# Optimization experiments

Measured on AMD Instinct MI355X. Metric: run time of the kernel, lower is better.

The kernel has to match this reference:

```python
import jax, jax.numpy as jnp
import numpy as np

DIM = 1024
HEADS = 16
HEAD_DIM = DIM // HEADS
SCALE = HEAD_DIM ** -0.5
KSIZES = (1, 3, 5)


def setup_inputs() -> dict:
    key = jax.random.key(0)
    ks = jax.random.split(key, 16)
    b, n = 2, 2048
    s = 0.02
    inp = {
        "x": jax.random.normal(ks[0], (b, n, DIM), jnp.float32),
        "Wq": jax.random.normal(ks[1], (DIM, DIM), jnp.float32) * s,
        "Wk": jax.random.normal(ks[2], (DIM, DIM), jnp.float32) * s,
        "Wv": jax.random.normal(ks[3], (DIM, DIM), jnp.float32) * s,
        "Wo": jax.random.normal(ks[4], (DIM, DIM), jnp.float32) * s,
        "bo": jnp.zeros((DIM,), jnp.float32),
        "temperature": jnp.ones((1, HEADS, 1, 1), jnp.float32),
        "head_weights": jnp.ones((1, HEADS, 1, 1), jnp.float32),
    }
    # grouped Conv1d kernels: (out_ch=DIM, in_ch_per_group=DIM//HEADS, k)
    for i, k in enumerate(KSIZES):
        inp[f"conv_w{k}"] = jax.random.normal(ks[5 + i], (DIM, DIM // HEADS, k), jnp.float32) * s
        inp[f"conv_b{k}"] = jnp.zeros((DIM,), jnp.float32)
    return inp


def _grouped_conv1d(x_bdn, w, b, k):
    # x_bdn: [b, dim, n]; w: [dim, dim//HEADS, k]; 'same' padding for odd k
    y = jax.lax.conv_general_dilated(
        x_bdn, w, window_strides=(1,), padding=[(k // 2, k // 2)],
        dimension_numbers=("NCH", "OIH", "NCH"), feature_group_count=HEADS)
    return y + b[None, :, None]


def reference(x, Wq, Wk, Wv, Wo, bo, temperature, head_weights,
              conv_w1, conv_b1, conv_w3, conv_b3, conv_w5, conv_b5):
    b, n, _ = x.shape
    split = lambda t: t.reshape(b, n, HEADS, HEAD_DIM).transpose(0, 2, 1, 3)  # b h n d
    q = split(x @ Wq.T)
    k = split(x @ Wk.T)
    v = split(x @ Wv.T)
    dots = jnp.einsum("bhnd,bhmd->bhnm", q, k) * SCALE * temperature
    attn = jax.nn.softmax(dots, axis=-1)
    attn = attn * jax.nn.softmax(head_weights, axis=1)
    out = jnp.einsum("bhnm,bhmd->bhnd", attn, v)
    out = out.transpose(0, 2, 1, 3).reshape(b, n, DIM)  # b n (h d)
    oc = out.transpose(0, 2, 1)  # b dim n
    conv_sum = (_grouped_conv1d(oc, conv_w1, conv_b1, 1)
                + _grouped_conv1d(oc, conv_w3, conv_b3, 3)
                + _grouped_conv1d(oc, conv_w5, conv_b5, 5))
    n_scales = float(len(KSIZES))
    out_combined = out + conv_sum.transpose(0, 2, 1) / n_scales
    return out_combined @ Wo.T + bo
```

## Files before the change

### kernel.cpp

```cpp
#include <hip/hip_runtime.h>

#define DIM 1024
#define HEADS 16
#define HD 64
#define BATCH 2
#define SEQ 2048
#define MROWS (BATCH * SEQ)

typedef short s16x8 __attribute__((ext_vector_type(8)));
typedef short s16x4 __attribute__((ext_vector_type(4)));
typedef float f32x4 __attribute__((ext_vector_type(4)));

__device__ __forceinline__ short f2bf(float f) {
  unsigned u = __builtin_bit_cast(unsigned, f);
  u = u + 0x7fffu + ((u >> 16) & 1u);
  return (short)(u >> 16);
}

__device__ __forceinline__ float bf2f(short s) {
  unsigned u = ((unsigned)(unsigned short)s) << 16;
  return __builtin_bit_cast(float, u);
}

__device__ __forceinline__ float fexp2(float x) { return __builtin_amdgcn_exp2f(x); }

__device__ __forceinline__ unsigned cvtpk(float lo, float hi) {
  unsigned r;
  asm("v_cvt_pk_bf16_f32 %0, %1, %2" : "=v"(r) : "v"(lo), "v"(hi));
  return r;
}

__device__ __forceinline__ void gload16(const void* g, void* l) {
  __builtin_amdgcn_global_load_lds((__attribute__((address_space(1))) void*)g,
                                   (__attribute__((address_space(3))) void*)l,
                                   16, 0, 0);
}

__global__ __launch_bounds__(256) void cvt_bf16(const float* __restrict__ in,
                                                short* __restrict__ out, int n4) {
  int i = blockIdx.x * 256 + threadIdx.x;
  if (i >= n4) return;
  f32x4 v = *(const f32x4*)(in + (size_t)i * 4);
  s16x4 o;
#pragma unroll
  for (int j = 0; j < 4; ++j) o[j] = f2bf(v[j]);
  *(s16x4*)(out + (size_t)i * 4) = o;
}

__global__ __launch_bounds__(256)
void cvt_w4(const float* __restrict__ a, const float* __restrict__ b,
            const float* __restrict__ c, const float* __restrict__ d,
            short* __restrict__ oa, short* __restrict__ ob, short* __restrict__ oc,
            short* __restrict__ od) {
  int k = blockIdx.y;
  const float* in = (k == 0) ? a : (k == 1) ? b : (k == 2) ? c : d;
  short* out = (k == 0) ? oa : (k == 1) ? ob : (k == 2) ? oc : od;
  int i = blockIdx.x * 256 + threadIdx.x;
  f32x4 v = *(const f32x4*)(in + (size_t)i * 4);
  s16x4 o;
#pragma unroll
  for (int j = 0; j < 4; ++j) o[j] = f2bf(v[j]);
  *(s16x4*)(out + (size_t)i * 4) = o;
}

#define QSTAGE(BUF, KT)                                                                \
  _Pragma("unroll") for (int i = 0; i < 2; ++i) {                                      \
    int cbase = i * 512 + wave * 64;                                                   \
    int c = cbase + lane;                                                              \
    int row = c >> 3;                                                                  \
    int cb = ((c ^ row) & 7) << 4;                                                     \
    gload16((const char*)A + ((size_t)(brow + row) * DIM + (KT)) * 2 + cb,             \
            (char*)&As[BUF][0][0] + cbase * 16);                                       \
    gload16((const char*)Bq + ((size_t)(bcol + row) * DIM + (KT)) * 2 + cb,            \
            (char*)&Bs[BUF][0][0][0] + cbase * 16);                                    \
    gload16((const char*)Bk + ((size_t)(bcol + row) * DIM + (KT)) * 2 + cb,            \
            (char*)&Bs[BUF][1][0][0] + cbase * 16);                                    \
    gload16((const char*)Bv + ((size_t)(bcol + row) * DIM + (KT)) * 2 + cb,            \
            (char*)&Bs[BUF][2][0][0] + cbase * 16);                                    \
  }

__global__ __launch_bounds__(512)
void qkv_fused(const short* __restrict__ A, const short* __restrict__ Bq,
               const short* __restrict__ Bk, const short* __restrict__ Bv,
               const float* __restrict__ scq, short* __restrict__ oq,
               short* __restrict__ ok, short* __restrict__ ov) {
  __shared__ __align__(16) short As[2][128][64];
  __shared__ __align__(16) short Bs[2][3][128][64];
  const int tid = threadIdx.x;
  const int lane = tid & 63, wave = tid >> 6;
  const int fr = lane & 15, fg = lane >> 4;
  const int wr = wave >> 1, wc = wave & 1;
  const int brow = blockIdx.y * 128, bcol = blockIdx.x * 128;

  int offA[2][2], offB[2][4];
#pragma unroll
  for (int kk = 0; kk < 2; ++kk) {
    int sw = ((kk * 4 + fg) ^ (fr & 7)) << 4;
#pragma unroll
    for (int m = 0; m < 2; ++m) offA[kk][m] = (wr * 32 + m * 16 + fr) * 128 + sw;
#pragma unroll
    for (int n = 0; n < 4; ++n) offB[kk][n] = (wc * 64 + n * 16 + fr) * 128 + sw;
  }

  f32x4 acc[3][2][4] = {};

  QSTAGE(0, 0);
  __syncthreads();

  for (int kt = 0; kt < DIM; kt += 64) {
    const int cur = (kt >> 6) & 1;
    if (kt + 64 < DIM) { QSTAGE(cur ^ 1, kt + 64); }
    const char* Ab = (const char*)&As[cur][0][0];
    const char* Bb = (const char*)&Bs[cur][0][0][0];
#pragma unroll
    for (int kk = 0; kk < 2; ++kk) {
      s16x8 af[2];
#pragma unroll
      for (int m = 0; m < 2; ++m) af[m] = *(const s16x8*)(Ab + offA[kk][m]);
#pragma unroll
      for (int z = 0; z < 3; ++z) {
        s16x8 bfr[4];
#pragma unroll
        for (int n = 0; n < 4; ++n) bfr[n] = *(const s16x8*)(Bb + z * 16384 + offB[kk][n]);
#pragma unroll
        for (int m = 0; m < 2; ++m)
#pragma unroll
          for (int n = 0; n < 4; ++n)
            acc[z][m][n] =
                __builtin_amdgcn_mfma_f32_16x16x32_bf16(af[m], bfr[n], acc[z][m][n], 0, 0, 0);
      }
    }
    __syncthreads();
  }

  const int hh = (bcol >> 6) + wc;
  const float sv = scq[hh];
#pragma unroll
  for (int m = 0; m < 2; ++m) {
#pragma unroll
    for (int n = 0; n < 4; ++n) {
      int i0 = brow + wr * 32 + m * 16 + fg * 4;
      int dd = n * 16 + fr;
#pragma unroll
      for (int r = 0; r < 4; ++r) {
        int i = i0 + r;
        size_t qko = (((size_t)(i >> 11) * HEADS + hh) * SEQ + (i & (SEQ - 1))) * HD + dd;
        oq[qko] = f2bf(acc[0][m][n][r] * sv);
        ok[qko] = f2bf(acc[1][m][n][r]);
      }
      s16x4 o4;
#pragma unroll
      for (int r = 0; r < 4; ++r) o4[r] = f2bf(acc[2][m][n][r]);
      *(s16x4*)&ov[(((size_t)(i0 >> 11) * HEADS + hh) * HD + dd) * SEQ + (i0 & (SEQ - 1))] = o4;
    }
  }
}

#define GSTAGE(BUF, KT)                                                              \
  _Pragma("unroll") for (int i = 0; i < 4; ++i) {                                    \
    int cbase = (wave * 4 + i) * 64;                                                 \
    int chunk = cbase + lane;                                                        \
    int row = chunk >> 3;                                                            \
    int cb = ((chunk ^ row) & 7) << 4;                                               \
    gload16((const char*)A + ((size_t)(brow + row) * DIM + (KT)) * 2 + cb,           \
            (char*)&As[BUF][0][0] + cbase * 16);                                     \
    gload16((const char*)Bw + ((size_t)(bcol + row) * DIM + (KT)) * 2 + cb,          \
            (char*)&Bs[BUF][0][0] + cbase * 16);                                     \
  }

__global__ __launch_bounds__(256)
void out_gemm(const short* __restrict__ A, const short* __restrict__ Bw,
              const float* __restrict__ bias, float* __restrict__ out) {
  __shared__ __align__(16) short As[2][128][64];
  __shared__ __align__(16) short Bs[2][128][64];
  const int tid = threadIdx.x;
  const int lane = tid & 63, wave = tid >> 6;
  const int fr = lane & 15, fg = lane >> 4;
  const int wr = wave >> 1, wc = wave & 1;
  const int brow = blockIdx.y * 128, bcol = blockIdx.x * 128;
  f32x4 acc[4][4] = {};

  int offA[2][4], offB[2][4];
#pragma unroll
  for (int kk = 0; kk < 2; ++kk)
#pragma unroll
    for (int f = 0; f < 4; ++f) {
      int sw = ((kk * 4 + fg) ^ (fr & 7)) << 4;
      offA[kk][f] = (wr * 64 + f * 16 + fr) * 128 + sw;
      offB[kk][f] = (wc * 64 + f * 16 + fr) * 128 + sw;
    }

  GSTAGE(0, 0);
  __syncthreads();

  for (int kt = 0; kt < DIM; kt += 64) {
    const int cur = (kt >> 6) & 1;
    if (kt + 64 < DIM) { GSTAGE(cur ^ 1, kt + 64); }
    const char* Ab = (const char*)&As[cur][0][0];
    const char* Bb = (const char*)&Bs[cur][0][0];
#pragma unroll
    for (int kk = 0; kk < 2; ++kk) {
      s16x8 af[4], bfr[4];
#pragma unroll
      for (int m = 0; m < 4; ++m) af[m] = *(const s16x8*)(Ab + offA[kk][m]);
#pragma unroll
      for (int n = 0; n < 4; ++n) bfr[n] = *(const s16x8*)(Bb + offB[kk][n]);
#pragma unroll
      for (int m = 0; m < 4; ++m)
#pragma unroll
        for (int n = 0; n < 4; ++n)
          acc[m][n] = __builtin_amdgcn_mfma_f32_16x16x32_bf16(af[m], bfr[n], acc[m][n], 0, 0, 0);
    }
    __syncthreads();
  }

#pragma unroll
  for (int m = 0; m < 4; ++m) {
#pragma unroll
    for (int n = 0; n < 4; ++n) {
      int i0 = brow + wr * 64 + m * 16 + fg * 4;
      int j = bcol + wc * 64 + n * 16 + fr;
#pragma unroll
      for (int r = 0; r < 4; ++r)
        out[(size_t)(i0 + r) * DIM + j] = acc[m][n][r] + bias[j];
    }
  }
}

#define STAGE(BUF, KT)                                                                   \
  gload16((const char*)K + (bhoff + (size_t)((KT) + srow) * HD) * 2 + scs,               \
          (char*)&Ks[BUF][0][0] + wbyte);                                                \
  gload16((const char*)Vt + (vbase + (size_t)srow * SEQ + (KT)) * 2 + scs,               \
          (char*)&Vs[BUF][0][0] + wbyte);

#define ATTN_TILE(CUR, STG, KTSTG, DOSTAGE, WAITSTR)                                     \
  {                                                                                      \
    asm volatile("s_waitcnt " WAITSTR ::: "memory");                                     \
    __builtin_amdgcn_s_barrier();                                                        \
    asm volatile("" ::: "memory");                                                       \
    if (DOSTAGE) { STAGE(STG, KTSTG); }                                                  \
    f32x4 st[4] = {};                                                                    \
    __builtin_amdgcn_s_setprio(1);                                                       \
    _Pragma("unroll") for (int ks = 0; ks < 2; ++ks) {                                   \
      _Pragma("unroll") for (int kf = 0; kf < 4; ++kf) {                                 \
        const s16x8 kfr = *(const s16x8*)((const char*)&Ks[CUR][0][0] + off[ks][kf]);    \
        st[kf] = __builtin_amdgcn_mfma_f32_16x16x32_bf16(kfr, qf_[ks], st[kf], 0, 0, 0); \
      }                                                                                  \
    }                                                                                    \
    __builtin_amdgcn_s_setprio(0);                                                       \
    float rsum = 0.f;                                                                    \
    _Pragma("unroll") for (int kf = 0; kf < 4; ++kf) {                                   \
      float p0 = fexp2(st[kf][0]), p1 = fexp2(st[kf][1]);                                \
      float p2 = fexp2(st[kf][2]), p3 = fexp2(st[kf][3]);                                \
      rsum += (p0 + p1) + (p2 + p3);                                                     \
      uint2 pk;                                                                          \
      pk.x = cvtpk(p0, p1);                                                              \
      pk.y = cvtpk(p2, p3);                                                              \
      *(uint2*)((char*)Psb + pwoff[kf]) = pk;                                            \
    }                                                                                    \
    lrow += rsum;                                                                        \
    __builtin_amdgcn_s_setprio(1);                                                       \
    _Pragma("unroll") for (int ks2 = 0; ks2 < 2; ++ks2) {                                \
      const s16x8 pfr = *(const s16x8*)((const char*)Psb + proff[ks2]);                  \
      _Pragma("unroll") for (int vf = 0; vf < 4; ++vf) {                                 \
        const s16x8 vfr = *(const s16x8*)((const char*)&Vs[CUR][0][0] + off[ks2][vf]);   \
        oacc[vf] = __builtin_amdgcn_mfma_f32_16x16x32_bf16(vfr, pfr, oacc[vf], 0, 0, 0); \
      }                                                                                  \
    }                                                                                    \
    __builtin_amdgcn_s_setprio(0);                                                       \
  }

__global__ __launch_bounds__(512)
void attn_fwd(const short* __restrict__ Q, const short* __restrict__ K,
              const short* __restrict__ Vt, short* __restrict__ att,
              const float* __restrict__ hw) {
  __shared__ __align__(16) short Ks[3][64][64];
  __shared__ __align__(16) short Vs[3][64][64];
  __shared__ __align__(16) short Ps[8][16][72];
  const int bh = blockIdx.y;
  const int h = bh & (HEADS - 1);
  const int qbase = blockIdx.x * 128;
  const int tid = threadIdx.x;
  const int lane = tid & 63, wave = tid >> 6;
  const int fr = lane & 15, fg = lane >> 4;
  const int frx = (fr & 7);

  float hmax = -1e30f;
  for (int i = 0; i < HEADS; ++i) hmax = fmaxf(hmax, hw[i]);
  float hsum = 0.f;
  for (int i = 0; i < HEADS; ++i) hsum += expf(hw[i] - hmax);
  const float hwsm = expf(hw[h] - hmax) / hsum;

  const size_t bhoff = (size_t)bh * SEQ * HD;
  const int qrow = qbase + wave * 16 + fr;
  s16x8 qf_[2];
#pragma unroll
  for (int ks = 0; ks < 2; ++ks)
    qf_[ks] = *(const s16x8*)&Q[bhoff + (size_t)qrow * HD + ks * 32 + fg * 8];

  int off[2][4];
#pragma unroll
  for (int ks = 0; ks < 2; ++ks)
#pragma unroll
    for (int f = 0; f < 4; ++f)
      off[ks][f] = (f * 16 + fr) * 128 + (((ks * 4 + fg) ^ frx) << 4);
  int pwoff[4], proff[2];
#pragma unroll
  for (int kf = 0; kf < 4; ++kf) pwoff[kf] = ((wave * 16 + fr) * 72 + kf * 16 + fg * 4) * 2;
#pragma unroll
  for (int ks2 = 0; ks2 < 2; ++ks2) proff[ks2] = ((wave * 16 + fr) * 72 + ks2 * 32 + fg * 8) * 2;
  const char* Psb = (const char*)&Ps[0][0][0];

  f32x4 oacc[4] = {};
  float lrow = 0.f;

  const int srow = tid >> 3;
  const int scs = ((tid & 7) ^ (srow & 7)) << 4;
  const int wbyte = wave * 64 * 16;
  const size_t vbase = (size_t)bh * HD * SEQ;

  STAGE(0, 0);
  STAGE(1, 64);

  for (int ktg = 0; ktg + 192 <= SEQ; ktg += 192) {
    ATTN_TILE(0, 2, ktg + 128, true, "vmcnt(2)");
    ATTN_TILE(1, 0, ktg + 192, true, "vmcnt(2)");
    ATTN_TILE(2, 1, ktg + 256, true, "vmcnt(2)");
  }
  ATTN_TILE(0, 0, 0, false, "vmcnt(2)");
  ATTN_TILE(1, 0, 0, false, "vmcnt(0)");

  lrow += __shfl_xor(lrow, 16);
  lrow += __shfl_xor(lrow, 32);

  const int b = bh >> 4;
  const float isc = hwsm / lrow;
#pragma unroll
  for (int vf = 0; vf < 4; ++vf) {
    s16x4 o4;
#pragma unroll
    for (int r = 0; r < 4; ++r) o4[r] = f2bf(oacc[vf][r] * isc);
    *(s16x4*)&att[((size_t)b * SEQ + qrow) * DIM + h * HD + vf * 16 + fg * 4] = o4;
  }
}

__global__ __launch_bounds__(256)
void prep_weff(const float* __restrict__ w1, const float* __restrict__ b1,
               const float* __restrict__ w3, const float* __restrict__ b3,
               const float* __restrict__ w5, const float* __restrict__ b5,
               const float* __restrict__ temp, short* __restrict__ weff,
               float* __restrict__ bsum, float* __restrict__ scq) {
  int idx = blockIdx.x * 256 + threadIdx.x;
  if (idx >= DIM * 64) return;
  float t0 = w5[(size_t)idx * 5 + 0];
  float t1 = w5[(size_t)idx * 5 + 1] + w3[(size_t)idx * 3 + 0];
  float t2 = w5[(size_t)idx * 5 + 2] + w3[(size_t)idx * 3 + 1] + w1[idx];
  float t3 = w5[(size_t)idx * 5 + 3] + w3[(size_t)idx * 3 + 2];
  float t4 = w5[(size_t)idx * 5 + 4];
  weff[0 * DIM * 64 + idx] = f2bf(t0);
  weff[1 * DIM * 64 + idx] = f2bf(t1);
  weff[2 * DIM * 64 + idx] = f2bf(t2);
  weff[3 * DIM * 64 + idx] = f2bf(t3);
  weff[4 * DIM * 64 + idx] = f2bf(t4);
  if ((idx & 63) == 0) {
    int o = idx >> 6;
    bsum[o] = b1[o] + b3[o] + b5[o];
  }
  if (idx < HEADS) scq[idx] = 0.125f * temp[idx] * 1.44269504f;
}

#define CP 68
__global__ __launch_bounds__(256)
void conv_mfma(const short* __restrict__ attb, const short* __restrict__ weff,
               const float* __restrict__ bsum, short* __restrict__ comb) {
  __shared__ __align__(16) short As[132][CP];
  __shared__ __align__(16) short Ws[5][64][CP];
  const int b = blockIdx.z, g = blockIdx.y, n0 = blockIdx.x * 128;
  const int tid = threadIdx.x, lane = tid & 63, wave = tid >> 6;
  const int fr = lane & 15, fg = lane >> 4;

  const short* abase = attb + (size_t)b * SEQ * DIM + g * 64;
  for (int idx = tid; idx < 132 * 8; idx += 256) {
    int r = idx >> 3, cb = (idx & 7) * 8;
    int rn = n0 + r - 2;
    s16x8 v = {};
    if (rn >= 0 && rn < SEQ) v = *(const s16x8*)&abase[(size_t)rn * DIM + cb];
    *(s16x8*)&As[r][cb] = v;
  }
  for (int idx = tid; idx < 5 * 64 * 8; idx += 256) {
    int t = idx >> 9;
    int rem = idx & 511;
    int o = rem >> 3, cb = (rem & 7) * 8;
    s16x8 v = *(const s16x8*)&weff[((size_t)t * DIM + g * 64 + o) * 64 + cb];
    *(s16x8*)&Ws[t][o][cb] = v;
  }
  __syncthreads();

  f32x4 acc[2][4] = {};
#pragma unroll
  for (int dt = 0; dt < 5; ++dt) {
#pragma unroll
    for (int kk = 0; kk < 2; ++kk) {
      const int ko = kk * 32 + fg * 8;
      s16x8 af[2], bfr[4];
#pragma unroll
      for (int m = 0; m < 2; ++m)
        af[m] = *(const s16x8*)&As[wave * 32 + m * 16 + fr + dt][ko];
#pragma unroll
      for (int n = 0; n < 4; ++n) bfr[n] = *(const s16x8*)&Ws[dt][n * 16 + fr][ko];
#pragma unroll
      for (int m = 0; m < 2; ++m)
#pragma unroll
        for (int n = 0; n < 4; ++n)
          acc[m][n] = __builtin_amdgcn_mfma_f32_16x16x32_bf16(af[m], bfr[n], acc[m][n], 0, 0, 0);
    }
  }

#pragma unroll
  for (int m = 0; m < 2; ++m) {
#pragma unroll
    for (int n = 0; n < 4; ++n) {
      int lrow0 = wave * 32 + m * 16 + fg * 4;
      int col = n * 16 + fr;
      float bs = bsum[g * 64 + col];
#pragma unroll
      for (int r = 0; r < 4; ++r) {
        int lr = lrow0 + r;
        float res = bf2f(As[lr + 2][col]);
        float outv = res + (acc[m][n][r] + bs) * (1.f / 3.f);
        comb[((size_t)b * SEQ + n0 + lr) * DIM + g * 64 + col] = f2bf(outv);
      }
    }
  }
}

extern "C" void kernel_launch(void* const* d_in, const int* in_sizes, int n_in, void* d_out,
                              int out_size, void* d_ws, size_t ws_size, hipStream_t stream) {
  const float* x = (const float*)d_in[0];
  const float* Wq = (const float*)d_in[1];
  const float* Wk = (const float*)d_in[2];
  const float* Wv = (const float*)d_in[3];
  const float* Wo = (const float*)d_in[4];
  const float* bo = (const float*)d_in[5];
  const float* temp = (const float*)d_in[6];
  const float* hw = (const float*)d_in[7];
  const float* w1 = (const float*)d_in[8];
  const float* b1 = (const float*)d_in[9];
  const float* w3 = (const float*)d_in[10];
  const float* b3 = (const float*)d_in[11];
  const float* w5 = (const float*)d_in[12];
  const float* b5 = (const float*)d_in[13];

  char* ws = (char*)d_ws;
  const size_t MB = 1u << 20;
  short* xb = (short*)(ws);
  short* wqb = (short*)(ws + 8 * MB);
  short* wkb = (short*)(ws + 10 * MB);
  short* wvb = (short*)(ws + 12 * MB);
  short* wob = (short*)(ws + 14 * MB);
  short* qb = (short*)(ws + 16 * MB);
  short* kb = (short*)(ws + 24 * MB);
  short* vtb = (short*)(ws + 32 * MB);
  short* attb = (short*)(ws + 40 * MB);
  short* comb = (short*)(ws + 48 * MB);
  short* weff = (short*)(ws + 56 * MB);
  float* bsum = (float*)(ws + 57 * MB);
  float* scq = (float*)(ws + 57 * MB + 4096);

  cvt_bf16<<<4096, 256, 0, stream>>>(x, xb, (MROWS * DIM) / 4);
  cvt_w4<<<dim3(1024, 4), 256, 0, stream>>>(Wq, Wk, Wv, Wo, wqb, wkb, wvb, wob);
  prep_weff<<<256, 256, 0, stream>>>(w1, b1, w3, b3, w5, b5, temp, weff, bsum, scq);

  qkv_fused<<<dim3(DIM / 128, MROWS / 128), 512, 0, stream>>>(xb, wqb, wkb, wvb, scq, qb, kb, vtb);

  attn_fwd<<<dim3(SEQ / 128, BATCH * HEADS), 512, 0, stream>>>(qb, kb, vtb, attb, hw);

  conv_mfma<<<dim3(SEQ / 128, HEADS, BATCH), 256, 0, stream>>>(attb, weff, bsum, comb);

  dim3 go(DIM / 128, MROWS / 128);
  out_gemm<<<go, 256, 0, stream>>>(comb, wob, bo, (float*)d_out);
}
```

Measured before the change: 124.6 us.

## Switch attention to 32x32x16 MFMA with in-register P via permlane swap

Rewrites the attention inner loop to use 32x32x16 bf16 MFMAs, with each wave owning 32 query rows, and halves the block to 256 threads. The softmax probabilities are repacked into the PV operand layout in registers using v_permlane32_swap instead of a round trip through an LDS P buffer, so the Ps shared array and its extra LDS reads and writes go away. Each thread now issues two K and two V staging loads per tile, and the vmcnt waits are adjusted to match. The cost is more accumulator registers per thread and scalar, non-vectorised output stores that need per-row scale shuffles.

New measurement: 124.1 us. About the same (-0.4%).

```diff
diff --git a/kernel.cpp b/kernel.cpp
--- a/kernel.cpp
+++ b/kernel.cpp
@@ -10,6 +10,8 @@
 typedef short s16x8 __attribute__((ext_vector_type(8)));
 typedef short s16x4 __attribute__((ext_vector_type(4)));
 typedef float f32x4 __attribute__((ext_vector_type(4)));
+typedef float f32x16 __attribute__((ext_vector_type(16)));
+typedef unsigned u32x4 __attribute__((ext_vector_type(4)));
 
 __device__ __forceinline__ short f2bf(float f) {
   unsigned u = __builtin_bit_cast(unsigned, f);
@@ -228,10 +230,43 @@
 }
 
 #define STAGE(BUF, KT)                                                                   \
-  gload16((const char*)K + (bhoff + (size_t)((KT) + srow) * HD) * 2 + scs,               \
-          (char*)&Ks[BUF][0][0] + wbyte);                                                \
-  gload16((const char*)Vt + (vbase + (size_t)srow * SEQ + (KT)) * 2 + scs,               \
-          (char*)&Vs[BUF][0][0] + wbyte);
+  gload16((const char*)K + (bhoff + (size_t)((KT) + srow0) * HD) * 2 + scs0,             \
+          (char*)&Ks[BUF][0][0] + wb0);                                                  \
+  gload16((const char*)K + (bhoff + (size_t)((KT) + srow1) * HD) * 2 + scs1,             \
+          (char*)&Ks[BUF][0][0] + wb1);                                                  \
+  gload16((const char*)Vt + (vbase + (size_t)srow0 * SEQ + (KT)) * 2 + scs0,             \
+          (char*)&Vs[BUF][0][0] + wb0);                                                  \
+  gload16((const char*)Vt + (vbase + (size_t)srow1 * SEQ + (KT)) * 2 + scs1,             \
+          (char*)&Vs[BUF][0][0] + wb1);
+
+#define SOFTPV(CUR, ST, KCB)                                                             \
+  {                                                                                      \
+    float p[16];                                                                         \
+    _Pragma("unroll") for (int r = 0; r < 16; ++r) p[r] = fexp2(ST[r]);                  \
+    lrow += ((p[0] + p[1]) + (p[2] + p[3])) + ((p[4] + p[5]) + (p[6] + p[7])) +          \
+            ((p[8] + p[9]) + (p[10] + p[11])) + ((p[12] + p[13]) + (p[14] + p[15]));     \
+    unsigned pk[8];                                                                      \
+    _Pragma("unroll") for (int q4 = 0; q4 < 4; ++q4) {                                   \
+      pk[q4 * 2] = cvtpk(p[q4 * 4 + 0], p[q4 * 4 + 1]);                                  \
+      pk[q4 * 2 + 1] = cvtpk(p[q4 * 4 + 2], p[q4 * 4 + 3]);                              \
+    }                                                                                    \
+    _Pragma("unroll") for (int kcl = 0; kcl < 2; ++kcl) {                                \
+      unsigned a0 = pk[kcl * 4 + 0], b0 = pk[kcl * 4 + 2];                               \
+      unsigned a1 = pk[kcl * 4 + 1], b1 = pk[kcl * 4 + 3];                               \
+      asm("v_permlane32_swap_b32 %0, %1" : "+v"(a0), "+v"(b0));                          \
+      asm("v_permlane32_swap_b32 %0, %1" : "+v"(a1), "+v"(b1));                          \
+      u32x4 pw;                                                                          \
+      pw.x = a0; pw.y = a1; pw.z = b0; pw.w = b1;                                        \
+      s16x8 pf = __builtin_bit_cast(s16x8, pw);                                          \
+      const char* vb = (const char*)&Vs[CUR][0][0] + off[(KCB) + kcl];                   \
+      s16x8 v0 = *(const s16x8*)vb;                                                      \
+      s16x8 v1 = *(const s16x8*)(vb + 4096);                                             \
+      __builtin_amdgcn_s_setprio(1);                                                     \
+      oacc0 = __builtin_amdgcn_mfma_f32_32x32x16_bf16(pf, v0, oacc0, 0, 0, 0);           \
+      oacc1 = __builtin_amdgcn_mfma_f32_32x32x16_bf16(pf, v1, oacc1, 0, 0, 0);           \
+      __builtin_amdgcn_s_setprio(0);                                                     \
+    }                                                                                    \
+  }
 
 #define ATTN_TILE(CUR, STG, KTSTG, DOSTAGE, WAITSTR)                                     \
   {                                                                                      \
@@ -239,51 +274,32 @@
     __builtin_amdgcn_s_barrier();                                                        \
     asm volatile("" ::: "memory");                                                       \
     if (DOSTAGE) { STAGE(STG, KTSTG); }                                                  \
-    f32x4 st[4] = {};                                                                    \
+    f32x16 st0 = {}, st1 = {};                                                           \
     __builtin_amdgcn_s_setprio(1);                                                       \
-    _Pragma("unroll") for (int ks = 0; ks < 2; ++ks) {                                   \
-      _Pragma("unroll") for (int kf = 0; kf < 4; ++kf) {                                 \
-        const s16x8 kfr = *(const s16x8*)((const char*)&Ks[CUR][0][0] + off[ks][kf]);    \
-        st[kf] = __builtin_amdgcn_mfma_f32_16x16x32_bf16(kfr, qf_[ks], st[kf], 0, 0, 0); \
-      }                                                                                  \
+    _Pragma("unroll") for (int dc = 0; dc < 4; ++dc) {                                   \
+      const char* kb = (const char*)&Ks[CUR][0][0] + off[dc];                            \
+      s16x8 k0 = *(const s16x8*)kb;                                                      \
+      s16x8 k1 = *(const s16x8*)(kb + 4096);                                             \
+      st0 = __builtin_amdgcn_mfma_f32_32x32x16_bf16(k0, qf[dc], st0, 0, 0, 0);           \
+      st1 = __builtin_amdgcn_mfma_f32_32x32x16_bf16(k1, qf[dc], st1, 0, 0, 0);           \
     }                                                                                    \
     __builtin_amdgcn_s_setprio(0);                                                       \
-    float rsum = 0.f;                                                                    \
-    _Pragma("unroll") for (int kf = 0; kf < 4; ++kf) {                                   \
-      float p0 = fexp2(st[kf][0]), p1 = fexp2(st[kf][1]);                                \
-      float p2 = fexp2(st[kf][2]), p3 = fexp2(st[kf][3]);                                \
-      rsum += (p0 + p1) + (p2 + p3);                                                     \
-      uint2 pk;                                                                          \
-      pk.x = cvtpk(p0, p1);                                                              \
-      pk.y = cvtpk(p2, p3);                                                              \
-      *(uint2*)((char*)Psb + pwoff[kf]) = pk;                                            \
-    }                                                                                    \
-    lrow += rsum;                                                                        \
-    __builtin_amdgcn_s_setprio(1);                                                       \
-    _Pragma("unroll") for (int ks2 = 0; ks2 < 2; ++ks2) {                                \
-      const s16x8 pfr = *(const s16x8*)((const char*)Psb + proff[ks2]);                  \
-      _Pragma("unroll") for (int vf = 0; vf < 4; ++vf) {                                 \
-        const s16x8 vfr = *(const s16x8*)((const char*)&Vs[CUR][0][0] + off[ks2][vf]);   \
-        oacc[vf] = __builtin_amdgcn_mfma_f32_16x16x32_bf16(vfr, pfr, oacc[vf], 0, 0, 0); \
-      }                                                                                  \
-    }                                                                                    \
-    __builtin_amdgcn_s_setprio(0);                                                       \
-  }
-
-__global__ __launch_bounds__(512)
+    SOFTPV(CUR, st0, 0);                                                                 \
+    SOFTPV(CUR, st1, 2);                                                                 \
+  }
+
+__global__ __launch_bounds__(256)
 void attn_fwd(const short* __restrict__ Q, const short* __restrict__ K,
               const short* __restrict__ Vt, short* __restrict__ att,
               const float* __restrict__ hw) {
   __shared__ __align__(16) short Ks[3][64][64];
   __shared__ __align__(16) short Vs[3][64][64];
-  __shared__ __align__(16) short Ps[8][16][72];
   const int bh = blockIdx.y;
   const int h = bh & (HEADS - 1);
   const int qbase = blockIdx.x * 128;
   const int tid = threadIdx.x;
   const int lane = tid & 63, wave = tid >> 6;
-  const int fr = lane & 15, fg = lane >> 4;
-  const int frx = (fr & 7);
+  const int l31 = lane & 31, hi = lane >> 5;
 
   float hmax = -1e30f;
   for (int i = 0; i < HEADS; ++i) hmax = fmaxf(hmax, hw[i]);
@@ -292,55 +308,50 @@
   const float hwsm = expf(hw[h] - hmax) / hsum;
 
   const size_t bhoff = (size_t)bh * SEQ * HD;
-  const int qrow = qbase + wave * 16 + fr;
-  s16x8 qf_[2];
-#pragma unroll
-  for (int ks = 0; ks < 2; ++ks)
-    qf_[ks] = *(const s16x8*)&Q[bhoff + (size_t)qrow * HD + ks * 32 + fg * 8];
-
-  int off[2][4];
-#pragma unroll
-  for (int ks = 0; ks < 2; ++ks)
-#pragma unroll
-    for (int f = 0; f < 4; ++f)
-      off[ks][f] = (f * 16 + fr) * 128 + (((ks * 4 + fg) ^ frx) << 4);
-  int pwoff[4], proff[2];
-#pragma unroll
-  for (int kf = 0; kf < 4; ++kf) pwoff[kf] = ((wave * 16 + fr) * 72 + kf * 16 + fg * 4) * 2;
-#pragma unroll
-  for (int ks2 = 0; ks2 < 2; ++ks2) proff[ks2] = ((wave * 16 + fr) * 72 + ks2 * 32 + fg * 8) * 2;
-  const char* Psb = (const char*)&Ps[0][0][0];
-
-  f32x4 oacc[4] = {};
+  const size_t vbase = (size_t)bh * HD * SEQ;
+  const int qrow = qbase + wave * 32 + l31;
+
+  s16x8 qf[4];
+#pragma unroll
+  for (int dc = 0; dc < 4; ++dc)
+    qf[dc] = *(const s16x8*)&Q[bhoff + (size_t)qrow * HD + dc * 16 + hi * 8];
+
+  int off[4];
+#pragma unroll
+  for (int c = 0; c < 4; ++c) off[c] = l31 * 128 + (((2 * c + hi) ^ (l31 & 7)) << 4);
+
+  const int c0 = wave * 64 + lane;
+  const int srow0 = c0 >> 3;
+  const int scs0 = ((c0 & 7) ^ (srow0 & 7)) << 4;
+  const int srow1 = srow0 + 32;
+  const int scs1 = ((c0 & 7) ^ (srow1 & 7)) << 4;
+  const int wb0 = wave * 1024, wb1 = 4096 + wave * 1024;
+
+  f32x16 oacc0 = {}, oacc1 = {};
   float lrow = 0.f;
-
-  const int srow = tid >> 3;
-  const int scs = ((tid & 7) ^ (srow & 7)) << 4;
-  const int wbyte = wave * 64 * 16;
-  const size_t vbase = (size_t)bh * HD * SEQ;
 
   STAGE(0, 0);
   STAGE(1, 64);
 
   for (int ktg = 0; ktg + 192 <= SEQ; ktg += 192) {
-    ATTN_TILE(0, 2, ktg + 128, true, "vmcnt(2)");
-    ATTN_TILE(1, 0, ktg + 192, true, "vmcnt(2)");
-    ATTN_TILE(2, 1, ktg + 256, true, "vmcnt(2)");
-  }
-  ATTN_TILE(0, 0, 0, false, "vmcnt(2)");
+    ATTN_TILE(0, 2, ktg + 128, true, "vmcnt(4)");
+    ATTN_TILE(1, 0, ktg + 192, true, "vmcnt(4)");
+    ATTN_TILE(2, 1, ktg + 256, true, "vmcnt(4)");
+  }
+  ATTN_TILE(0, 0, 0, false, "vmcnt(4)");
   ATTN_TILE(1, 0, 0, false, "vmcnt(0)");
 
-  lrow += __shfl_xor(lrow, 16);
   lrow += __shfl_xor(lrow, 32);
 
   const int b = bh >> 4;
   const float isc = hwsm / lrow;
 #pragma unroll
-  for (int vf = 0; vf < 4; ++vf) {
-    s16x4 o4;
-#pragma unroll
-    for (int r = 0; r < 4; ++r) o4[r] = f2bf(oacc[vf][r] * isc);
-    *(s16x4*)&att[((size_t)b * SEQ + qrow) * DIM + h * HD + vf * 16 + fg * 4] = o4;
+  for (int reg = 0; reg < 16; ++reg) {
+    int q = (reg & 3) + 8 * (reg >> 2) + 4 * hi;
+    float sc = __shfl(isc, q);
+    size_t ro = ((size_t)b * SEQ + qbase + wave * 32 + q) * DIM + h * HD;
+    att[ro + l31] = f2bf(oacc0[reg] * sc);
+    att[ro + 32 + l31] = f2bf(oacc1[reg] * sc);
   }
 }
 
@@ -473,7 +484,7 @@
 
   qkv_fused<<<dim3(DIM / 128, MROWS / 128), 512, 0, stream>>>(xb, wqb, wkb, wvb, scq, qb, kb, vtb);
 
-  attn_fwd<<<dim3(SEQ / 128, BATCH * HEADS), 512, 0, stream>>>(qb, kb, vtb, attb, hw);
+  attn_fwd<<<dim3(SEQ / 128, BATCH * HEADS), 256, 0, stream>>>(qb, kb, vtb, attb, hw);
 
   conv_mfma<<<dim3(SEQ / 128, HEADS, BATCH), 256, 0, stream>>>(attb, weff, bsum, comb);
 
```
